# Kernel optimization log

Hardware: AMD Instinct MI355X
Metric: run time of the kernel (lower is better)

The kernel has to match this reference:

```python
import jax, jax.numpy as jnp
import numpy as np

PILLAR_GROUPS = [[0,1,2],[3,4],[5,6],[7,8,9],[10,11],[12,13,14],[15,16],[17,18],[19],[20,21,22],[23,24,25],[26,27,28]]
N_GROUPS = len(PILLAR_GROUPS)      # 12
MAX_G = max(len(g) for g in PILLAR_GROUPS)  # 3
ENC_DIM = 8
EPS = 1e-5

# static padded gather indices + validity mask so all 12 encoders run in one einsum
_idx = np.zeros((N_GROUPS, MAX_G), np.int32)
_msk = np.zeros((N_GROUPS, MAX_G), np.float32)
for _i, _g in enumerate(PILLAR_GROUPS):
    _idx[_i, :len(_g)] = _g
    _msk[_i, :len(_g)] = 1.0
IDX = jnp.asarray(_idx)
MASK = jnp.asarray(_msk)


def bn(h, gamma, beta, mean, var):
    # BatchNorm1d in eval mode (running statistics)
    return gamma * (h - mean) * jax.lax.rsqrt(var + EPS) + beta


def setup_inputs() -> dict:
    key = jax.random.key(0)
    ks = jax.random.split(key, 40)
    B = 524288

    def rn(k, shape, s=0.2):
        return jax.random.normal(k, shape, jnp.float32) * s

    def bn_params(k, d):
        k1, k2, k3, k4 = jax.random.split(k, 4)
        return (1.0 + rn(k1, (d,), 0.05),          # gamma
                rn(k2, (d,), 0.05),                 # beta
                rn(k3, (d,), 0.1),                  # running_mean
                0.5 + jax.random.uniform(k4, (d,), jnp.float32))  # running_var > 0

    g1, bb1, m1, v1 = bn_params(ks[10], 64)
    g2, bb2, m2, v2 = bn_params(ks[11], 32)
    g3, bb3, m3, v3 = bn_params(ks[12], 16)
    eg, ebt, em, ev = bn_params(ks[13], ENC_DIM)
    # per-encoder BN params: [12, 8]
    eg = jnp.tile(eg, (N_GROUPS, 1)) + rn(ks[14], (N_GROUPS, ENC_DIM), 0.02)
    ebt = jnp.tile(ebt, (N_GROUPS, 1)) + rn(ks[15], (N_GROUPS, ENC_DIM), 0.02)
    em = jnp.tile(em, (N_GROUPS, 1)) + rn(ks[16], (N_GROUPS, ENC_DIM), 0.02)
    ev = jnp.tile(ev, (N_GROUPS, 1)) + 0.1 * jax.random.uniform(ks[17], (N_GROUPS, ENC_DIM))

    return {
        "x": jax.random.normal(ks[0], (B, 29), jnp.float32),
        "We": rn(ks[1], (N_GROUPS, MAX_G, ENC_DIM)),  # padded; pad rows hit zeroed x
        "be": rn(ks[2], (N_GROUPS, ENC_DIM)),
        "enc_gamma": eg, "enc_beta": ebt, "enc_mean": em, "enc_var": ev,
        "Wa": rn(ks[3], (ENC_DIM * N_GROUPS, N_GROUPS)),
        "ba": rn(ks[4], (N_GROUPS,)),
        "W1": rn(ks[5], (ENC_DIM * N_GROUPS, 64)), "b1": rn(ks[6], (64,)),
        "g1": g1, "bb1": bb1, "m1": m1, "v1": v1,
        "W2": rn(ks[7], (64, 32)), "b2": rn(ks[8], (32,)),
        "g2": g2, "bb2": bb2, "m2": m2, "v2": v2,
        "W3": rn(ks[9], (32, 16)), "b3": rn(ks[18], (16,)),
        "g3": g3, "bb3": bb3, "m3": m3, "v3": v3,
        "W4": rn(ks[19], (16, 1)), "b4": rn(ks[20], (1,)),
    }


def reference(x, We, be, enc_gamma, enc_beta, enc_mean, enc_var,
              Wa, ba, W1, b1, g1, bb1, m1, v1,
              W2, b2, g2, bb2, m2, v2,
              W3, b3, g3, bb3, m3, v3, W4, b4):
    B = x.shape[0]
    # gather each pillar group (padded to MAX_G, pads zeroed) -> [B, 12, 3]
    xg = x[:, IDX] * MASK
    # all 12 encoders: Linear + ReLU + BN(eval)  -> reps [B, 12, 8]
    reps = jax.nn.relu(jnp.einsum('bgi,gio->bgo', xg, We) + be)
    reps = bn(reps, enc_gamma, enc_beta, enc_mean, enc_var)
    stacked = reps.reshape(B, -1)                      # [B, 96] (cat order matches)
    weights = jax.nn.softmax(stacked @ Wa + ba, axis=1)  # [B, 12]
    attended = (reps * weights[:, :, None]).reshape(B, -1)  # [B, 96]
    h = bn(jax.nn.relu(attended @ W1 + b1), g1, bb1, m1, v1)  # dropout = identity (eval)
    h = bn(jax.nn.relu(h @ W2 + b2), g2, bb2, m2, v2)
    h = bn(jax.nn.relu(h @ W3 + b3), g3, bb3, m3, v3)
    return jax.nn.sigmoid(h @ W4 + b4)[:, 0]           # squeeze(1) -> [B]
```

## Files before the change

### kernel.cpp

```cpp
#include <hip/hip_runtime.h>
#include <math.h>


typedef _Float16 f16x8 __attribute__((ext_vector_type(8)));
typedef float    f32x4 __attribute__((ext_vector_type(4)));

#define EPS 1e-5f

__device__ __forceinline__ float rcp_fast(float v) { return __builtin_amdgcn_rcpf(v); }

template<int N>
__device__ __forceinline__ float dpp_ror(float v) {
    return __int_as_float(__builtin_amdgcn_update_dpp(
        0, __float_as_int(v), 0x120 + N, 0xF, 0xF, true));
}
__device__ __forceinline__ float row_sum16(float v) {
    v += dpp_ror<1>(v); v += dpp_ror<2>(v); v += dpp_ror<4>(v); v += dpp_ror<8>(v);
    return v;
}
__device__ __forceinline__ float row_max16(float v) {
    v = fmaxf(v, dpp_ror<1>(v)); v = fmaxf(v, dpp_ror<2>(v));
    v = fmaxf(v, dpp_ror<4>(v)); v = fmaxf(v, dpp_ror<8>(v));
    return v;
}

__host__ __device__ constexpr unsigned long long packGS() {
    constexpr int gs[12] = {0,3,5,7,10,12,15,17,19,20,23,26};
    unsigned long long v = 0;
    for (int g = 0; g < 12; ++g) v |= (unsigned long long)gs[g] << (5*g);
    return v;
}
__host__ __device__ constexpr unsigned packGL() {
    constexpr int gl[12] = {3,2,2,3,2,3,2,2,1,3,3,3};
    unsigned v = 0;
    for (int g = 0; g < 12; ++g) v |= (unsigned)gl[g] << (2*g);
    return v;
}

__global__ __launch_bounds__(256, 2) void fused_kernel(
    const float* __restrict__ x,
    const float* __restrict__ We,  const float* __restrict__ be,
    const float* __restrict__ eg,  const float* __restrict__ ebt,
    const float* __restrict__ em,  const float* __restrict__ ev,
    const float* __restrict__ Wa,  const float* __restrict__ ba,
    const float* __restrict__ W1,  const float* __restrict__ b1,
    const float* __restrict__ g1,  const float* __restrict__ bb1,
    const float* __restrict__ m1,  const float* __restrict__ v1,
    const float* __restrict__ W2,  const float* __restrict__ b2,
    const float* __restrict__ g2,  const float* __restrict__ bb2,
    const float* __restrict__ m2,  const float* __restrict__ v2,
    const float* __restrict__ W3,  const float* __restrict__ b3,
    const float* __restrict__ g3,  const float* __restrict__ bb3,
    const float* __restrict__ m3,  const float* __restrict__ v3,
    const float* __restrict__ W4,  const float* __restrict__ b4,
    float* __restrict__ out, int B, int ntiles)
{
    __shared__ __align__(16) char smem_raw[53760];
    const int lane = threadIdx.x & 63;
    const int wave = threadIdx.x >> 6;
    const int l15  = lane & 15;
    const int quad = lane >> 4;

    _Float16* repT[2]; float* wT[2]; _Float16* h1T[2]; _Float16* h2T[2];
    #pragma unroll
    for (int u = 0; u < 2; ++u) {
        char* sw = smem_raw + wave * 13440 + u * 6720;
        repT[u] = (_Float16*)sw;
        wT[u]   = (float*)   (sw + 3328);
        h1T[u]  = (_Float16*)(sw + 4416);
        h2T[u]  = (_Float16*)sw;
    }

    constexpr unsigned long long GS = packGS();
    constexpr unsigned GL = packGL();

    f16x8 Benc[6];
    #pragma unroll
    for (int t = 0; t < 6; ++t) {
        const int n = t*16 + l15;
        const int g = n >> 3, o = n & 7;
        const int gs = (int)((GS >> (5*g)) & 31);
        const int gl = (int)((GL >> (2*g)) & 3);
        #pragma unroll
        for (int j = 0; j < 8; ++j) {
            const int k  = quad*8 + j;
            const int ji = k - gs;
            float v = (ji >= 0 && ji < gl) ? We[(g*3 + ji)*8 + o] : 0.f;
            Benc[t][j] = (_Float16)v;
        }
    }
    f16x8 Bwa[3];
    #pragma unroll
    for (int s = 0; s < 3; ++s)
        #pragma unroll
        for (int j = 0; j < 8; ++j) {
            const int k = s*32 + quad*8 + j;
            Bwa[s][j] = (_Float16)((l15 < 12) ? Wa[k*12 + l15] : 0.f);
        }
    f16x8 Bw1[12];
    #pragma unroll
    for (int t = 0; t < 4; ++t)
        #pragma unroll
        for (int s = 0; s < 3; ++s)
            #pragma unroll
            for (int j = 0; j < 8; ++j) {
                const int k = s*32 + quad*8 + j;
                Bw1[t*3 + s][j] = (_Float16)W1[k*64 + t*16 + l15];
            }
    f16x8 Bw2[4];
    #pragma unroll
    for (int t = 0; t < 2; ++t)
        #pragma unroll
        for (int s = 0; s < 2; ++s)
            #pragma unroll
            for (int j = 0; j < 8; ++j) {
                const int k = s*32 + quad*8 + j;
                Bw2[t*2 + s][j] = (_Float16)W2[k*32 + t*16 + l15];
            }
    f16x8 Bw3;
    #pragma unroll
    for (int j = 0; j < 8; ++j)
        Bw3[j] = (_Float16)W3[(quad*8 + j)*16 + l15];

    float encB[6], encS[6], encT[6];
    #pragma unroll
    for (int t = 0; t < 6; ++t) {
        const int c = t*16 + l15;
        float s = eg[c] * rsqrtf(ev[c] + EPS);
        encS[t] = s; encT[t] = ebt[c] - em[c]*s; encB[t] = be[c];
    }
    const float baL = (l15 < 12) ? ba[l15] : -1e4f;
    float b1L[4], s1L[4], t1L[4];
    #pragma unroll
    for (int t = 0; t < 4; ++t) {
        const int c = t*16 + l15;
        float s = g1[c] * rsqrtf(v1[c] + EPS);
        s1L[t] = s; t1L[t] = bb1[c] - m1[c]*s; b1L[t] = b1[c];
    }
    float b2L[2], s2L[2], t2L[2];
    #pragma unroll
    for (int t = 0; t < 2; ++t) {
        const int c = t*16 + l15;
        float s = g2[c] * rsqrtf(v2[c] + EPS);
        s2L[t] = s; t2L[t] = bb2[c] - m2[c]*s; b2L[t] = b2[c];
    }
    const float sv3 = g3[l15] * rsqrtf(v3[l15] + EPS);
    const float b3L = b3[l15], s3L = sv3, t3L = bb3[l15] - m3[l15]*sv3;
    const float w4L = W4[l15];
    const float b4v = b4[0];

    const int tbase = blockIdx.x * 32 + wave * 2;

    auto loadx = [&](int pp, float (&xv)[2][8]) {
        #pragma unroll
        for (int u = 0; u < 2; ++u) {
            int tl = tbase + 8*pp + u; if (tl > ntiles-1) tl = ntiles-1;
            int xr = tl*16 + l15;      if (xr > B-1)      xr = B-1;
            const float* xp = x + (size_t)xr*29 + quad*8;
            if (quad < 3) {
                #pragma unroll
                for (int j = 0; j < 8; ++j) xv[u][j] = xp[j];
            } else {
                #pragma unroll
                for (int j = 0; j < 5; ++j) xv[u][j] = xp[j];
                xv[u][5] = xv[u][6] = xv[u][7] = 0.f;
            }
        }
    };

    float xcur[2][8];
    loadx(0, xcur);

    #pragma unroll 1
    for (int p = 0; p < 4; ++p) {
        float xnext[2][8];
        loadx(p < 3 ? p + 1 : 3, xnext);

        f16x8 ax[2];
        #pragma unroll
        for (int u = 0; u < 2; ++u)
            #pragma unroll
            for (int j = 0; j < 8; ++j) ax[u][j] = (_Float16)xcur[u][j];

        #pragma unroll
        for (int u = 0; u < 2; ++u)
            #pragma unroll
            for (int t = 0; t < 6; ++t) {
                f32x4 c = { encB[t], encB[t], encB[t], encB[t] };
                c = __builtin_amdgcn_mfma_f32_16x16x32_f16(ax[u], Benc[t], c, 0, 0, 0);
                #pragma unroll
                for (int r = 0; r < 4; ++r)
                    repT[u][(quad*4 + r)*104 + t*16 + l15] =
                        (_Float16)fmaf(fmaxf(c[r], 0.f), encS[t], encT[t]);
            }

        f16x8 afr[2][3];
        #pragma unroll
        for (int u = 0; u < 2; ++u)
            #pragma unroll
            for (int s = 0; s < 3; ++s)
                afr[u][s] = *(const f16x8*)(repT[u] + l15*104 + s*32 + quad*8);

        #pragma unroll
        for (int u = 0; u < 2; ++u) {
            f32x4 c2 = { baL, baL, baL, baL };
            #pragma unroll
            for (int s = 0; s < 3; ++s)
                c2 = __builtin_amdgcn_mfma_f32_16x16x32_f16(afr[u][s], Bwa[s], c2, 0, 0, 0);
            #pragma unroll
            for (int r = 0; r < 4; ++r) {
                float v  = c2[r];
                float mx = row_max16(v);
                float e  = __expf(v - mx);
                float sm = row_sum16(e);
                wT[u][(quad*4 + r)*17 + l15] = e * rcp_fast(sm);
            }
        }

        #pragma unroll
        for (int u = 0; u < 2; ++u) {
            f32x4 c3[4];
            #pragma unroll
            for (int t = 0; t < 4; ++t) c3[t] = { b1L[t], b1L[t], b1L[t], b1L[t] };
            #pragma unroll
            for (int s = 0; s < 3; ++s) {
                _Float16 wh = (_Float16)wT[u][l15*17 + s*4 + quad];
                f16x8 aw;
                #pragma unroll
                for (int j = 0; j < 8; ++j) aw[j] = afr[u][s][j] * wh;
                #pragma unroll
                for (int t = 0; t < 4; ++t)
                    c3[t] = __builtin_amdgcn_mfma_f32_16x16x32_f16(aw, Bw1[t*3 + s], c3[t], 0, 0, 0);
            }
            #pragma unroll
            for (int t = 0; t < 4; ++t)
                #pragma unroll
                for (int r = 0; r < 4; ++r)
                    h1T[u][(quad*4 + r)*72 + t*16 + l15] =
                        (_Float16)fmaf(fmaxf(c3[t][r], 0.f), s1L[t], t1L[t]);
        }

        #pragma unroll
        for (int u = 0; u < 2; ++u) {
            f32x4 c4[2];
            #pragma unroll
            for (int t = 0; t < 2; ++t) c4[t] = { b2L[t], b2L[t], b2L[t], b2L[t] };
            #pragma unroll
            for (int s = 0; s < 2; ++s) {
                f16x8 a = *(const f16x8*)(h1T[u] + l15*72 + s*32 + quad*8);
                #pragma unroll
                for (int t = 0; t < 2; ++t)
                    c4[t] = __builtin_amdgcn_mfma_f32_16x16x32_f16(a, Bw2[t*2 + s], c4[t], 0, 0, 0);
            }
            #pragma unroll
            for (int t = 0; t < 2; ++t)
                #pragma unroll
                for (int r = 0; r < 4; ++r)
                    h2T[u][(quad*4 + r)*40 + t*16 + l15] =
                        (_Float16)fmaf(fmaxf(c4[t][r], 0.f), s2L[t], t2L[t]);
        }

        #pragma unroll
        for (int u = 0; u < 2; ++u) {
            f32x4 c5 = { b3L, b3L, b3L, b3L };
            f16x8 a = *(const f16x8*)(h2T[u] + l15*40 + quad*8);
            c5 = __builtin_amdgcn_mfma_f32_16x16x32_f16(a, Bw3, c5, 0, 0, 0);

            float z[4];
            #pragma unroll
            for (int r = 0; r < 4; ++r) {
                float v = fmaf(fmaxf(c5[r], 0.f), s3L, t3L);
                z[r] = row_sum16(v * w4L);
            }
            const int tl = tbase + 8*p + u;
            if (l15 == 0 && tl < ntiles) {
                float4 o;
                o.x = rcp_fast(1.f + __expf(-(z[0] + b4v)));
                o.y = rcp_fast(1.f + __expf(-(z[1] + b4v)));
                o.z = rcp_fast(1.f + __expf(-(z[2] + b4v)));
                o.w = rcp_fast(1.f + __expf(-(z[3] + b4v)));
                *(float4*)(out + tl*16 + quad*4) = o;
            }
        }

        #pragma unroll
        for (int u = 0; u < 2; ++u)
            #pragma unroll
            for (int j = 0; j < 8; ++j) xcur[u][j] = xnext[u][j];
    }
}

extern "C" void kernel_launch(void* const* d_in, const int* in_sizes, int n_in,
                              void* d_out, int out_size, void* d_ws, size_t ws_size,
                              hipStream_t stream)
{
    const float* x   = (const float*)d_in[0];
    const float* We  = (const float*)d_in[1];
    const float* be  = (const float*)d_in[2];
    const float* eg  = (const float*)d_in[3];
    const float* ebt = (const float*)d_in[4];
    const float* em  = (const float*)d_in[5];
    const float* ev  = (const float*)d_in[6];
    const float* Wa  = (const float*)d_in[7];
    const float* ba  = (const float*)d_in[8];
    const float* W1  = (const float*)d_in[9];
    const float* b1  = (const float*)d_in[10];
    const float* g1  = (const float*)d_in[11];
    const float* bb1 = (const float*)d_in[12];
    const float* m1  = (const float*)d_in[13];
    const float* v1  = (const float*)d_in[14];
    const float* W2  = (const float*)d_in[15];
    const float* b2  = (const float*)d_in[16];
    const float* g2  = (const float*)d_in[17];
    const float* bb2 = (const float*)d_in[18];
    const float* m2  = (const float*)d_in[19];
    const float* v2  = (const float*)d_in[20];
    const float* W3  = (const float*)d_in[21];
    const float* b3  = (const float*)d_in[22];
    const float* g3  = (const float*)d_in[23];
    const float* bb3 = (const float*)d_in[24];
    const float* m3  = (const float*)d_in[25];
    const float* v3  = (const float*)d_in[26];
    const float* W4  = (const float*)d_in[27];
    const float* b4  = (const float*)d_in[28];

    const int B = in_sizes[0] / 29;
    const int ntiles = (B + 15) / 16;
    const int blocks = (ntiles + 31) / 32;

    fused_kernel<<<blocks, 256, 0, stream>>>(
        x, We, be, eg, ebt, em, ev, Wa, ba,
        W1, b1, g1, bb1, m1, v1,
        W2, b2, g2, bb2, m2, v2,
        W3, b3, g3, bb3, m3, v3,
        W4, b4, (float*)d_out, B, ntiles);
}
```

Before: 235.1 us.

## Permute intermediate layouts for packed LDS stores and process one tile per iteration

Each iteration now handles a single 16-row tile instead of two interleaved tiles, with 8 iterations per wave. Shared memory per wave shrinks from 13440 to 8000 bytes. The weight matrices are loaded with permuted K indices so the encoder, layer-1 and layer-2 outputs can be written to LDS as packed f16x2/f16x4 stores through cvt_pkrtz, instead of scalar half stores. This cuts LDS store instructions and LDS footprint, but it removes the two-tile interleaving that gave the MFMA chains independent work, so latency hiding may be reduced. A bounds-checked tail path for the output store is also added.

```diff
diff --git a/kernel.cpp b/kernel.cpp
--- a/kernel.cpp
+++ b/kernel.cpp
@@ -3,11 +3,17 @@
 
 
 typedef _Float16 f16x8 __attribute__((ext_vector_type(8)));
+typedef _Float16 f16x4 __attribute__((ext_vector_type(4)));
+typedef _Float16 f16x2 __attribute__((ext_vector_type(2)));
 typedef float    f32x4 __attribute__((ext_vector_type(4)));
 
 #define EPS 1e-5f
 
 __device__ __forceinline__ float rcp_fast(float v) { return __builtin_amdgcn_rcpf(v); }
+
+__device__ __forceinline__ f16x2 pkrtz(float a, float b) {
+    return __builtin_bit_cast(f16x2, __builtin_amdgcn_cvt_pkrtz(a, b));
+}
 
 template<int N>
 __device__ __forceinline__ float dpp_ror(float v) {
@@ -22,6 +28,16 @@
     v = fmaxf(v, dpp_ror<1>(v)); v = fmaxf(v, dpp_ror<2>(v));
     v = fmaxf(v, dpp_ror<4>(v)); v = fmaxf(v, dpp_ror<8>(v));
     return v;
+}
+
+__device__ __forceinline__ int perm96(int k) {
+    return ((k >> 5) + 3 * (k & 1)) * 16 + ((k & 31) >> 1);
+}
+__device__ __forceinline__ int perm64(int k) {
+    return (k & 3) * 16 + (k >> 2);
+}
+__device__ __forceinline__ int perm32(int k) {
+    return (k & 1) * 16 + (k >> 1);
 }
 
 __host__ __device__ constexpr unsigned long long packGS() {
@@ -55,21 +71,18 @@
     const float* __restrict__ W4,  const float* __restrict__ b4,
     float* __restrict__ out, int B, int ntiles)
 {
-    __shared__ __align__(16) char smem_raw[53760];
+    __shared__ __align__(16) char smem_raw[32000];
     const int lane = threadIdx.x & 63;
     const int wave = threadIdx.x >> 6;
     const int l15  = lane & 15;
     const int quad = lane >> 4;
-
-    _Float16* repT[2]; float* wT[2]; _Float16* h1T[2]; _Float16* h2T[2];
-    #pragma unroll
-    for (int u = 0; u < 2; ++u) {
-        char* sw = smem_raw + wave * 13440 + u * 6720;
-        repT[u] = (_Float16*)sw;
-        wT[u]   = (float*)   (sw + 3328);
-        h1T[u]  = (_Float16*)(sw + 4416);
-        h2T[u]  = (_Float16*)sw;
-    }
+    const int qh   = quad >> 1;
+
+    char* sw = smem_raw + wave * 8000;
+    _Float16* rep = (_Float16*)sw;
+    float*    wTb = (float*)   (sw + 3328);
+    _Float16* h1b = (_Float16*)(sw + 4416);
+    _Float16* h2b = (_Float16*)(sw + 6720);
 
     constexpr unsigned long long GS = packGS();
     constexpr unsigned GL = packGL();
@@ -85,8 +98,7 @@
         for (int j = 0; j < 8; ++j) {
             const int k  = quad*8 + j;
             const int ji = k - gs;
-            float v = (ji >= 0 && ji < gl) ? We[(g*3 + ji)*8 + o] : 0.f;
-            Benc[t][j] = (_Float16)v;
+            Benc[t][j] = (_Float16)((ji >= 0 && ji < gl) ? We[(g*3 + ji)*8 + o] : 0.f);
         }
     }
     f16x8 Bwa[3];
@@ -94,8 +106,8 @@
     for (int s = 0; s < 3; ++s)
         #pragma unroll
         for (int j = 0; j < 8; ++j) {
-            const int k = s*32 + quad*8 + j;
-            Bwa[s][j] = (_Float16)((l15 < 12) ? Wa[k*12 + l15] : 0.f);
+            const int n = perm96(s*32 + quad*8 + j);
+            Bwa[s][j] = (_Float16)((l15 < 12) ? Wa[n*12 + l15] : 0.f);
         }
     f16x8 Bw1[12];
     #pragma unroll
@@ -104,8 +116,8 @@
         for (int s = 0; s < 3; ++s)
             #pragma unroll
             for (int j = 0; j < 8; ++j) {
-                const int k = s*32 + quad*8 + j;
-                Bw1[t*3 + s][j] = (_Float16)W1[k*64 + t*16 + l15];
+                const int n = perm96(s*32 + quad*8 + j);
+                Bw1[t*3 + s][j] = (_Float16)W1[n*64 + t*16 + l15];
             }
     f16x8 Bw2[4];
     #pragma unroll
@@ -114,13 +126,13 @@
         for (int s = 0; s < 2; ++s)
             #pragma unroll
             for (int j = 0; j < 8; ++j) {
-                const int k = s*32 + quad*8 + j;
-                Bw2[t*2 + s][j] = (_Float16)W2[k*32 + t*16 + l15];
+                const int n = perm64(s*32 + quad*8 + j);
+                Bw2[t*2 + s][j] = (_Float16)W2[n*32 + t*16 + l15];
             }
     f16x8 Bw3;
     #pragma unroll
     for (int j = 0; j < 8; ++j)
-        Bw3[j] = (_Float16)W3[(quad*8 + j)*16 + l15];
+        Bw3[j] = (_Float16)W3[perm32(quad*8 + j)*16 + l15];
 
     float encB[6], encS[6], encT[6];
     #pragma unroll
@@ -149,121 +161,119 @@
     const float w4L = W4[l15];
     const float b4v = b4[0];
 
-    const int tbase = blockIdx.x * 32 + wave * 2;
-
-    auto loadx = [&](int pp, float (&xv)[2][8]) {
-        #pragma unroll
-        for (int u = 0; u < 2; ++u) {
-            int tl = tbase + 8*pp + u; if (tl > ntiles-1) tl = ntiles-1;
-            int xr = tl*16 + l15;      if (xr > B-1)      xr = B-1;
-            const float* xp = x + (size_t)xr*29 + quad*8;
-            if (quad < 3) {
-                #pragma unroll
-                for (int j = 0; j < 8; ++j) xv[u][j] = xp[j];
-            } else {
-                #pragma unroll
-                for (int j = 0; j < 5; ++j) xv[u][j] = xp[j];
-                xv[u][5] = xv[u][6] = xv[u][7] = 0.f;
-            }
+    auto loadx = [&](int tl, float (&xv)[8]) {
+        if (tl > ntiles-1) tl = ntiles-1;
+        int xr = tl*16 + l15; if (xr > B-1) xr = B-1;
+        const float* xp = x + (size_t)xr*29 + quad*8;
+        if (quad < 3) {
+            #pragma unroll
+            for (int j = 0; j < 8; ++j) xv[j] = xp[j];
+        } else {
+            #pragma unroll
+            for (int j = 0; j < 5; ++j) xv[j] = xp[j];
+            xv[5] = xv[6] = xv[7] = 0.f;
         }
     };
 
-    float xcur[2][8];
-    loadx(0, xcur);
+    int tile = blockIdx.x * 32 + wave;
+    float xf[8];
+    loadx(tile, xf);
 
     #pragma unroll 1
-    for (int p = 0; p < 4; ++p) {
-        float xnext[2][8];
-        loadx(p < 3 ? p + 1 : 3, xnext);
-
-        f16x8 ax[2];
-        #pragma unroll
-        for (int u = 0; u < 2; ++u)
-            #pragma unroll
-            for (int j = 0; j < 8; ++j) ax[u][j] = (_Float16)xcur[u][j];
-
-        #pragma unroll
-        for (int u = 0; u < 2; ++u)
-            #pragma unroll
-            for (int t = 0; t < 6; ++t) {
-                f32x4 c = { encB[t], encB[t], encB[t], encB[t] };
-                c = __builtin_amdgcn_mfma_f32_16x16x32_f16(ax[u], Benc[t], c, 0, 0, 0);
-                #pragma unroll
-                for (int r = 0; r < 4; ++r)
-                    repT[u][(quad*4 + r)*104 + t*16 + l15] =
-                        (_Float16)fmaf(fmaxf(c[r], 0.f), encS[t], encT[t]);
-            }
-
-        f16x8 afr[2][3];
-        #pragma unroll
-        for (int u = 0; u < 2; ++u)
+    for (int p = 0; p < 8; ++p) {
+        const int tnext = (p < 7) ? tile + 4 : tile;
+        float xn[8];
+        loadx(tnext, xn);
+
+        f16x8 ax;
+        #pragma unroll
+        for (int j = 0; j < 8; ++j) ax[j] = (_Float16)xf[j];
+
+        #pragma unroll
+        for (int tp = 0; tp < 3; ++tp) {
+            f32x4 ca = { encB[tp],   encB[tp],   encB[tp],   encB[tp]   };
+            f32x4 cb = { encB[tp+3], encB[tp+3], encB[tp+3], encB[tp+3] };
+            ca = __builtin_amdgcn_mfma_f32_16x16x32_f16(ax, Benc[tp],   ca, 0, 0, 0);
+            cb = __builtin_amdgcn_mfma_f32_16x16x32_f16(ax, Benc[tp+3], cb, 0, 0, 0);
+            #pragma unroll
+            for (int r = 0; r < 4; ++r) {
+                float va = fmaf(fmaxf(ca[r], 0.f), encS[tp],   encT[tp]);
+                float vb = fmaf(fmaxf(cb[r], 0.f), encS[tp+3], encT[tp+3]);
+                *(f16x2*)(rep + (quad*4 + r)*104 + tp*32 + l15*2) = pkrtz(va, vb);
+            }
+        }
+
+        f16x8 afr[3];
+        #pragma unroll
+        for (int s = 0; s < 3; ++s)
+            afr[s] = *(const f16x8*)(rep + l15*104 + s*32 + quad*8);
+
+        {
+            f32x4 c2 = { baL, baL, baL, baL };
             #pragma unroll
             for (int s = 0; s < 3; ++s)
-                afr[u][s] = *(const f16x8*)(repT[u] + l15*104 + s*32 + quad*8);
-
-        #pragma unroll
-        for (int u = 0; u < 2; ++u) {
-            f32x4 c2 = { baL, baL, baL, baL };
-            #pragma unroll
-            for (int s = 0; s < 3; ++s)
-                c2 = __builtin_amdgcn_mfma_f32_16x16x32_f16(afr[u][s], Bwa[s], c2, 0, 0, 0);
+                c2 = __builtin_amdgcn_mfma_f32_16x16x32_f16(afr[s], Bwa[s], c2, 0, 0, 0);
             #pragma unroll
             for (int r = 0; r < 4; ++r) {
                 float v  = c2[r];
                 float mx = row_max16(v);
                 float e  = __expf(v - mx);
                 float sm = row_sum16(e);
-                wT[u][(quad*4 + r)*17 + l15] = e * rcp_fast(sm);
-            }
-        }
-
-        #pragma unroll
-        for (int u = 0; u < 2; ++u) {
+                wTb[(quad*4 + r)*17 + l15] = e * rcp_fast(sm);
+            }
+        }
+
+        {
             f32x4 c3[4];
             #pragma unroll
             for (int t = 0; t < 4; ++t) c3[t] = { b1L[t], b1L[t], b1L[t], b1L[t] };
             #pragma unroll
             for (int s = 0; s < 3; ++s) {
-                _Float16 wh = (_Float16)wT[u][l15*17 + s*4 + quad];
-                f16x8 aw;
-                #pragma unroll
-                for (int j = 0; j < 8; ++j) aw[j] = afr[u][s][j] * wh;
+                float we = wTb[l15*17 + 2*s + qh];
+                float wo = wTb[l15*17 + 2*s + 6 + qh];
+                f16x2 wpk = pkrtz(we, wo);
+                f16x8 wv = { wpk[0], wpk[1], wpk[0], wpk[1],
+                             wpk[0], wpk[1], wpk[0], wpk[1] };
+                f16x8 aw = afr[s] * wv;
                 #pragma unroll
                 for (int t = 0; t < 4; ++t)
                     c3[t] = __builtin_amdgcn_mfma_f32_16x16x32_f16(aw, Bw1[t*3 + s], c3[t], 0, 0, 0);
             }
             #pragma unroll
-            for (int t = 0; t < 4; ++t)
-                #pragma unroll
-                for (int r = 0; r < 4; ++r)
-                    h1T[u][(quad*4 + r)*72 + t*16 + l15] =
-                        (_Float16)fmaf(fmaxf(c3[t][r], 0.f), s1L[t], t1L[t]);
-        }
-
-        #pragma unroll
-        for (int u = 0; u < 2; ++u) {
+            for (int r = 0; r < 4; ++r) {
+                float v0 = fmaf(fmaxf(c3[0][r], 0.f), s1L[0], t1L[0]);
+                float v1_ = fmaf(fmaxf(c3[1][r], 0.f), s1L[1], t1L[1]);
+                float v2_ = fmaf(fmaxf(c3[2][r], 0.f), s1L[2], t1L[2]);
+                float v3_ = fmaf(fmaxf(c3[3][r], 0.f), s1L[3], t1L[3]);
+                f16x2 p0 = pkrtz(v0,  v1_);
+                f16x2 p1 = pkrtz(v2_, v3_);
+                f16x4 pk = { p0[0], p0[1], p1[0], p1[1] };
+                *(f16x4*)(h1b + (quad*4 + r)*72 + l15*4) = pk;
+            }
+        }
+
+        {
             f32x4 c4[2];
             #pragma unroll
             for (int t = 0; t < 2; ++t) c4[t] = { b2L[t], b2L[t], b2L[t], b2L[t] };
             #pragma unroll
             for (int s = 0; s < 2; ++s) {
-                f16x8 a = *(const f16x8*)(h1T[u] + l15*72 + s*32 + quad*8);
+                f16x8 a = *(const f16x8*)(h1b + l15*72 + s*32 + quad*8);
                 #pragma unroll
                 for (int t = 0; t < 2; ++t)
                     c4[t] = __builtin_amdgcn_mfma_f32_16x16x32_f16(a, Bw2[t*2 + s], c4[t], 0, 0, 0);
             }
             #pragma unroll
-            for (int t = 0; t < 2; ++t)
-                #pragma unroll
-                for (int r = 0; r < 4; ++r)
-                    h2T[u][(quad*4 + r)*40 + t*16 + l15] =
-                        (_Float16)fmaf(fmaxf(c4[t][r], 0.f), s2L[t], t2L[t]);
-        }
-
-        #pragma unroll
-        for (int u = 0; u < 2; ++u) {
+            for (int r = 0; r < 4; ++r) {
+                float v0 = fmaf(fmaxf(c4[0][r], 0.f), s2L[0], t2L[0]);
+                float v1_ = fmaf(fmaxf(c4[1][r], 0.f), s2L[1], t2L[1]);
+                *(f16x2*)(h2b + (quad*4 + r)*40 + l15*2) = pkrtz(v0, v1_);
+            }
+        }
+
+        {
             f32x4 c5 = { b3L, b3L, b3L, b3L };
-            f16x8 a = *(const f16x8*)(h2T[u] + l15*40 + quad*8);
+            f16x8 a = *(const f16x8*)(h2b + l15*40 + quad*8);
             c5 = __builtin_amdgcn_mfma_f32_16x16x32_f16(a, Bw3, c5, 0, 0, 0);
 
             float z[4];
@@ -272,21 +282,27 @@
                 float v = fmaf(fmaxf(c5[r], 0.f), s3L, t3L);
                 z[r] = row_sum16(v * w4L);
             }
-            const int tl = tbase + 8*p + u;
-            if (l15 == 0 && tl < ntiles) {
-                float4 o;
-                o.x = rcp_fast(1.f + __expf(-(z[0] + b4v)));
-                o.y = rcp_fast(1.f + __expf(-(z[1] + b4v)));
-                o.z = rcp_fast(1.f + __expf(-(z[2] + b4v)));
-                o.w = rcp_fast(1.f + __expf(-(z[3] + b4v)));
-                *(float4*)(out + tl*16 + quad*4) = o;
-            }
-        }
-
-        #pragma unroll
-        for (int u = 0; u < 2; ++u)
-            #pragma unroll
-            for (int j = 0; j < 8; ++j) xcur[u][j] = xnext[u][j];
+            if (l15 == 0 && tile < ntiles) {
+                const int row = tile*16 + quad*4;
+                if (row + 3 < B) {
+                    float4 o;
+                    o.x = rcp_fast(1.f + __expf(-(z[0] + b4v)));
+                    o.y = rcp_fast(1.f + __expf(-(z[1] + b4v)));
+                    o.z = rcp_fast(1.f + __expf(-(z[2] + b4v)));
+                    o.w = rcp_fast(1.f + __expf(-(z[3] + b4v)));
+                    *(float4*)(out + row) = o;
+                } else {
+                    #pragma unroll
+                    for (int r = 0; r < 4; ++r)
+                        if (row + r < B)
+                            out[row + r] = rcp_fast(1.f + __expf(-(z[r] + b4v)));
+                }
+            }
+        }
+
+        tile = tnext;
+        #pragma unroll
+        for (int j = 0; j < 8; ++j) xf[j] = xn[j];
     }
 }
 
```

Result: faster. 212.2 us (-9.8%).
